# Optimization experiments

Measured on AMD Instinct MI355X. Metric: run time of the kernel, lower is better.

The kernel has to match this reference:

```python
import jax, jax.numpy as jnp
import numpy as np

# Each of the 16 differentiable binary logic ops op_k(a,b) is a polynomial
# c0 + ca*a + cb*b + cab*(a*b). Rows follow the standard difflogic op table
# (op 3 = 'a' pass-through, matching the residual init in the source).
_OP2POLY = np.array([
    [0, 0, 0, 0],    # 0: False
    [0, 0, 0, 1],    # 1: a AND b
    [0, 1, 0, -1],   # 2: a AND NOT b
    [0, 1, 0, 0],    # 3: a
    [0, 0, 1, -1],   # 4: NOT a AND b
    [0, 0, 1, 0],    # 5: b
    [0, 1, 1, -2],   # 6: XOR
    [0, 1, 1, -1],   # 7: OR
    [1, -1, -1, 1],  # 8: NOR
    [1, -1, -1, 2],  # 9: XNOR
    [1, 0, -1, 0],   # 10: NOT b
    [1, 0, -1, 1],   # 11: a OR NOT b
    [1, -1, 0, 0],   # 12: NOT a
    [1, -1, 0, 1],   # 13: NOT a OR b
    [1, 0, 0, -1],   # 14: NAND
    [1, 0, 0, 0],    # 15: True
], dtype=np.float32)

KERNEL_SIZE, STRIDE, PADDING, GROUPS, TREE_DEPTH, TAU = 3, 1, 1, 1, 4, 1.0


def setup_inputs() -> dict:
    key = jax.random.key(0)
    k0, k1, k2, k3, k4 = jax.random.split(key, 5)
    B, Cin, H, W = 16, 64, 64, 64
    OC, N = 128, 2 ** TREE_DEPTH
    x = jax.random.uniform(k0, (B, Cin, H, W), dtype=jnp.float32)
    weights = jax.random.normal(k1, (OC, N - 1, 16), dtype=jnp.float32)
    ci = jax.random.randint(k2, (OC, N), 0, Cin // GROUPS, dtype=jnp.int32)
    px = jax.random.randint(k3, (OC, N), 0, KERNEL_SIZE, dtype=jnp.int32)
    py = jax.random.randint(k4, (OC, N), 0, KERNEL_SIZE, dtype=jnp.int32)
    return {"x": x, "weights": weights, "input_channel_indices": ci,
            "input_pos_x_indices": px, "input_pos_y_indices": py}


def _forward(x, weights, ci, px, py):
    B, Cin, H, W = x.shape
    OC = weights.shape[0]
    N = 2 ** TREE_DEPTH
    # Training-mode weights with straight-through estimator:
    # value = one_hot(argmax), gradient flows through softmax.
    w_soft = jax.nn.softmax(weights / TAU, axis=-1).astype(x.dtype)
    w_hard = jax.nn.one_hot(jnp.argmax(weights, axis=-1), 16, dtype=x.dtype)
    w = w_soft + jax.lax.stop_gradient(w_hard - w_soft)
    # [OC, num_gates, 4] polynomial coefficients over (1, a, b, ab)
    coeffs = jnp.einsum('ogk,kc->ogc', w, jnp.asarray(_OP2POLY, x.dtype))

    xp = jnp.pad(x, ((0, 0), (0, 0), (PADDING, PADDING), (PADDING, PADDING)))
    oh = (H + 2 * PADDING - KERNEL_SIZE) // STRIDE + 1
    ow = (W + 2 * PADDING - KERNEL_SIZE) // STRIDE + 1

    icpg = Cin // GROUPS
    group_of_oc = jnp.arange(OC, dtype=jnp.int32) // (OC // GROUPS)
    chan = group_of_oc[:, None] * icpg + ci                       # [OC, N]
    rows = (jnp.arange(oh, dtype=jnp.int32) * STRIDE)[None, None, :] + py[:, :, None]  # [OC,N,oh]
    cols = (jnp.arange(ow, dtype=jnp.int32) * STRIDE)[None, None, :] + px[:, :, None]  # [OC,N,ow]
    # Irregular per-output gather: [B, OC, N, oh, ow]
    vals = xp[:, chan[:, :, None, None], rows[:, :, :, None], cols[:, :, None, :]]

    # Binary tree of logic gates, level by level (gates stored leaf-level first).
    gate_off = 0
    for _ in range(TREE_DEPTH):
        n = vals.shape[2] // 2
        a, b = vals[:, :, 0::2], vals[:, :, 1::2]
        cc = coeffs[:, gate_off:gate_off + n]                     # [OC, n, 4]
        c0, ca, cb, cab = (cc[None, :, :, i, None, None] for i in range(4))
        vals = c0 + ca * a + cb * b + cab * (a * b)
        gate_off += n
    y = vals[:, :, 0]                                             # [B, OC, oh, ow]

    # 2x2 OR-pool (soft OR = 1 - prod(1 - v)), floor division of spatial dims.
    ph, pw = oh // 2, ow // 2
    y = y[:, :, :ph * 2, :pw * 2].reshape(B, OC, ph, 2, pw, 2)
    return 1.0 - jnp.prod(1.0 - y, axis=(3, 5))


def reference(x, weights, input_channel_indices, input_pos_x_indices, input_pos_y_indices):
    return _forward(x, weights, input_channel_indices, input_pos_x_indices, input_pos_y_indices)
```

## Files before the change

kernel.cpp:

```cpp
#include <hip/hip_runtime.h>

#define BATCH 16
#define CIN   64
#define H_    64
#define W_    64
#define IMG   (H_ * W_)
#define OCH   128
#define NLEAF 16
#define NGATE 15
#define PH    32
#define PW    32

#define ROWS   6
#define RSTR   66
#define CHSTR  (ROWS * RSTR)
#define XSB    2
#define OPS_F  25348
#define DS_F   (OPS_F + OCH * 4)
#define SMEM_F (DS_F + OCH * NLEAF)

typedef float f4v __attribute__((ext_vector_type(4)));

__device__ __constant__ __align__(16) float OP2POLY[16][4] = {
    {0, 0, 0, 0}, {0, 0, 0, 1}, {0, 1, 0, -1}, {0, 1, 0, 0},
    {0, 0, 1, -1}, {0, 0, 1, 0}, {0, 1, 1, -2}, {0, 1, 1, -1},
    {1, -1, -1, 1}, {1, -1, -1, 2}, {1, 0, -1, 0}, {1, 0, -1, 1},
    {1, -1, 0, 0}, {1, -1, 0, 1}, {1, 0, 0, -1}, {1, 0, 0, 0}};

static __device__ __forceinline__ int rfl_i(int v) {
    return __builtin_amdgcn_readfirstlane(v);
}

__global__ __launch_bounds__(1024, 4) void logic_tree_fused(
    const float* __restrict__ x,
    const float* __restrict__ weights,
    const int* __restrict__ ci,
    const int* __restrict__ px,
    const int* __restrict__ py,
    float* __restrict__ out)
{
    __shared__ float smem[SMEM_F];
    int* smem_i = (int*)smem;
    unsigned char* smem_b = (unsigned char*)smem;

    const int blk = blockIdx.x;
    const int xcd = blk & 7;
    const int j   = blk >> 3;
    const int b   = (xcd << 1) | (j >> 4);
    const int strip = j & 15;
    const int r0  = strip << 2;
    const int tid = threadIdx.x;

    const float2* xb2 =
        reinterpret_cast<const float2*>(x + (size_t)b * (CIN * IMG));
#pragma unroll
    for (int i = 0; i < 12; ++i) {
        int f   = tid + i * 1024;
        int ch  = f / 192;
        int rem = f - ch * 192;
        int row = rem >> 5;
        int c2  = rem & 31;
        int gr  = r0 - 1 + row;
        float2 val = make_float2(0.f, 0.f);
        if ((unsigned)gr < (unsigned)H_)
            val = xb2[((ch << 6) | gr) * 32 + c2];
        *reinterpret_cast<float2*>(&smem[XSB + ch * CHSTR + row * RSTR + c2 * 2]) = val;
    }
    if (tid < 770) {
        int idx = (tid < 768) ? (XSB + (tid >> 1) * RSTR + 64 + (tid & 1))
                              : (tid - 768);
        smem[idx] = 0.0f;
    }
    for (int t = tid; t < OCH * NGATE; t += 1024) {
        const float4* wp4 = reinterpret_cast<const float4*>(weights + t * 16);
        const float4 a0 = wp4[0], a1 = wp4[1], a2 = wp4[2], a3 = wp4[3];
        const float wv[16] = {a0.x, a0.y, a0.z, a0.w, a1.x, a1.y, a1.z, a1.w,
                              a2.x, a2.y, a2.z, a2.w, a3.x, a3.y, a3.z, a3.w};
        int best = 0;
        float bv = wv[0];
#pragma unroll
        for (int k = 1; k < 16; ++k)
            if (wv[k] > bv) { bv = wv[k]; best = k; }
        int oc = t / 15, g = t - oc * 15;
        smem_b[OPS_F * 4 + oc * 16 + g] = (unsigned char)best;
        if (g == 14) smem_b[OPS_F * 4 + oc * 16 + 15] = 0;
    }
    for (int t = tid; t < OCH * NLEAF; t += 1024)
        smem_i[DS_F + t] = XSB + ci[t] * CHSTR + py[t] * RSTR + px[t] - 1;
    __syncthreads();

    const int wave = tid >> 6;
    const int lane = tid & 63;
    const size_t obase0 =
        (((size_t)b * OCH) * PH + (strip << 1) + (lane & 1)) * PW + (lane >> 1);

#pragma unroll 1
    for (int q = 0; q < 8; ++q) {
        const int oc = wave * 8 + q;

        const uint4 opsv = *reinterpret_cast<const uint4*>(&smem[OPS_F + oc * 4]);
        const unsigned ou[4] = {
            (unsigned)rfl_i((int)opsv.x), (unsigned)rfl_i((int)opsv.y),
            (unsigned)rfl_i((int)opsv.z), (unsigned)rfl_i((int)opsv.w)};

        int base[NLEAF];
        const int4* D4 = reinterpret_cast<const int4*>(smem_i + DS_F + oc * NLEAF);
#pragma unroll
        for (int m = 0; m < 4; ++m) {
            const int4 d = D4[m];
            base[4 * m + 0] = d.x + lane;
            base[4 * m + 1] = d.y + lane;
            base[4 * m + 2] = d.z + lane;
            base[4 * m + 3] = d.w + lane;
        }

        f4v v[NLEAF];
#pragma unroll
        for (int n = 0; n < NLEAF; ++n) {
            v[n].x = smem[base[n]];
            v[n].y = smem[base[n] + RSTR];
            v[n].z = smem[base[n] + 2 * RSTR];
            v[n].w = smem[base[n] + 3 * RSTR];
        }

        int go = 0;
#pragma unroll
        for (int lev = 8; lev >= 1; lev >>= 1) {
#pragma unroll
            for (int t = 0; t < lev; ++t) {
                const int g  = go + t;
                const int op = (int)((ou[g >> 2] >> ((g & 3) * 8)) & 255u);
                const float4 cc = reinterpret_cast<const float4*>(OP2POLY)[op];
                f4v a  = v[2 * t];
                f4v bb = v[2 * t + 1];
                v[t] = cc.x + cc.y * a + cc.z * bb + cc.w * (a * bb);
            }
            go += lev;
        }

        float p0 = (1.0f - v[0].x) * (1.0f - v[0].y);
        float p1 = (1.0f - v[0].z) * (1.0f - v[0].w);
        float q0 = p0 * __shfl_xor(p0, 1, 64);
        float q1 = p1 * __shfl_xor(p1, 1, 64);
        float val = (lane & 1) ? (1.0f - q1) : (1.0f - q0);
        out[obase0 + (size_t)oc * (PH * PW)] = val;
    }
}

extern "C" void kernel_launch(void* const* d_in, const int* in_sizes, int n_in,
                              void* d_out, int out_size, void* d_ws, size_t ws_size,
                              hipStream_t stream) {
    const float* x       = (const float*)d_in[0];
    const float* weights = (const float*)d_in[1];
    const int*   ci      = (const int*)d_in[2];
    const int*   px      = (const int*)d_in[3];
    const int*   py      = (const int*)d_in[4];
    float* out = (float*)d_out;
    (void)d_ws; (void)ws_size;

    logic_tree_fused<<<BATCH * 16, 1024, 0, stream>>>(x, weights, ci, px, py, out);
}
```

Before: 91.96 us.

## Halve row strip per block and double grid with 512-thread blocks

Each block now computes a 2-row output strip (one pooled row) instead of 4, so it stages 4 input rows per channel instead of 6 and needs less LDS. The grid doubles to 512 blocks of 512 threads, and each wave handles 16 output channels with 2-element vectors. This raises block count and occupancy at the cost of more redundant halo loads and repeated weight argmax decoding per block. Only even lanes write output, which halves the store width.

After: 96.56 us. +5.0%, slower.

```diff
diff --git a/kernel.cpp b/kernel.cpp
--- a/kernel.cpp
+++ b/kernel.cpp
@@ -11,15 +11,15 @@
 #define PH    32
 #define PW    32
 
-#define ROWS   6
+#define SROWS  4
 #define RSTR   66
-#define CHSTR  (ROWS * RSTR)
+#define CHSTR  (SROWS * RSTR)
 #define XSB    2
-#define OPS_F  25348
+#define OPS_F  16900
 #define DS_F   (OPS_F + OCH * 4)
 #define SMEM_F (DS_F + OCH * NLEAF)
 
-typedef float f4v __attribute__((ext_vector_type(4)));
+typedef float f2 __attribute__((ext_vector_type(2)));
 
 __device__ __constant__ __align__(16) float OP2POLY[16][4] = {
     {0, 0, 0, 0}, {0, 0, 0, 1}, {0, 1, 0, -1}, {0, 1, 0, 0},
@@ -31,7 +31,7 @@
     return __builtin_amdgcn_readfirstlane(v);
 }
 
-__global__ __launch_bounds__(1024, 4) void logic_tree_fused(
+__global__ __launch_bounds__(512, 4) void logic_tree_fused(
     const float* __restrict__ x,
     const float* __restrict__ weights,
     const int* __restrict__ ci,
@@ -46,57 +46,62 @@
     const int blk = blockIdx.x;
     const int xcd = blk & 7;
     const int j   = blk >> 3;
-    const int b   = (xcd << 1) | (j >> 4);
-    const int strip = j & 15;
-    const int r0  = strip << 2;
+    const int b   = (xcd << 1) | (j >> 5);
+    const int strip = j & 31;
+    const int r0  = strip << 1;
     const int tid = threadIdx.x;
 
     const float2* xb2 =
         reinterpret_cast<const float2*>(x + (size_t)b * (CIN * IMG));
 #pragma unroll
-    for (int i = 0; i < 12; ++i) {
-        int f   = tid + i * 1024;
-        int ch  = f / 192;
-        int rem = f - ch * 192;
-        int row = rem >> 5;
-        int c2  = rem & 31;
-        int gr  = r0 - 1 + row;
-        float2 val = make_float2(0.f, 0.f);
-        if ((unsigned)gr < (unsigned)H_)
-            val = xb2[((ch << 6) | gr) * 32 + c2];
-        *reinterpret_cast<float2*>(&smem[XSB + ch * CHSTR + row * RSTR + c2 * 2]) = val;
+    for (int i = 0; i < 17; ++i) {
+        int f = tid + i * 512;
+        if (f < 8448) {
+            int ch  = f / 132;
+            int rem = f - ch * 132;
+            int row = rem / 33;
+            int c2  = rem - row * 33;
+            int gr  = r0 - 1 + row;
+            float2 val = make_float2(0.f, 0.f);
+            if (c2 < 32 && (unsigned)gr < (unsigned)H_)
+                val = xb2[((ch << 6) | gr) * 32 + c2];
+            *reinterpret_cast<float2*>(
+                &smem[XSB + ch * CHSTR + row * RSTR + c2 * 2]) = val;
+        }
     }
-    if (tid < 770) {
-        int idx = (tid < 768) ? (XSB + (tid >> 1) * RSTR + 64 + (tid & 1))
-                              : (tid - 768);
-        smem[idx] = 0.0f;
+    if (tid < 2) smem[tid] = 0.0f;
+
+#pragma unroll
+    for (int i = 0; i < 4; ++i) {
+        int t = tid + i * 512;
+        if (t < OCH * NGATE) {
+            const float4* wp4 = reinterpret_cast<const float4*>(weights + t * 16);
+            const float4 a0 = wp4[0], a1 = wp4[1], a2 = wp4[2], a3 = wp4[3];
+            const float wv[16] = {a0.x, a0.y, a0.z, a0.w, a1.x, a1.y, a1.z, a1.w,
+                                  a2.x, a2.y, a2.z, a2.w, a3.x, a3.y, a3.z, a3.w};
+            int best = 0;
+            float bv = wv[0];
+#pragma unroll
+            for (int k = 1; k < 16; ++k)
+                if (wv[k] > bv) { bv = wv[k]; best = k; }
+            int oc = t / 15, g = t - oc * 15;
+            smem_b[OPS_F * 4 + oc * 16 + g] = (unsigned char)best;
+            if (g == 14) smem_b[OPS_F * 4 + oc * 16 + 15] = 0;
+        }
     }
-    for (int t = tid; t < OCH * NGATE; t += 1024) {
-        const float4* wp4 = reinterpret_cast<const float4*>(weights + t * 16);
-        const float4 a0 = wp4[0], a1 = wp4[1], a2 = wp4[2], a3 = wp4[3];
-        const float wv[16] = {a0.x, a0.y, a0.z, a0.w, a1.x, a1.y, a1.z, a1.w,
-                              a2.x, a2.y, a2.z, a2.w, a3.x, a3.y, a3.z, a3.w};
-        int best = 0;
-        float bv = wv[0];
 #pragma unroll
-        for (int k = 1; k < 16; ++k)
-            if (wv[k] > bv) { bv = wv[k]; best = k; }
-        int oc = t / 15, g = t - oc * 15;
-        smem_b[OPS_F * 4 + oc * 16 + g] = (unsigned char)best;
-        if (g == 14) smem_b[OPS_F * 4 + oc * 16 + 15] = 0;
+    for (int i = 0; i < 4; ++i) {
+        int t = tid + i * 512;
+        smem_i[DS_F + t] = XSB + ci[t] * CHSTR + py[t] * RSTR + px[t] - 1;
     }
-    for (int t = tid; t < OCH * NLEAF; t += 1024)
-        smem_i[DS_F + t] = XSB + ci[t] * CHSTR + py[t] * RSTR + px[t] - 1;
     __syncthreads();
 
     const int wave = tid >> 6;
     const int lane = tid & 63;
-    const size_t obase0 =
-        (((size_t)b * OCH) * PH + (strip << 1) + (lane & 1)) * PW + (lane >> 1);
 
 #pragma unroll 1
-    for (int q = 0; q < 8; ++q) {
-        const int oc = wave * 8 + q;
+    for (int q = 0; q < 16; ++q) {
+        const int oc = wave * 16 + q;
 
         const uint4 opsv = *reinterpret_cast<const uint4*>(&smem[OPS_F + oc * 4]);
         const unsigned ou[4] = {
@@ -114,13 +119,11 @@
             base[4 * m + 3] = d.w + lane;
         }
 
-        f4v v[NLEAF];
+        f2 v[NLEAF];
 #pragma unroll
         for (int n = 0; n < NLEAF; ++n) {
             v[n].x = smem[base[n]];
             v[n].y = smem[base[n] + RSTR];
-            v[n].z = smem[base[n] + 2 * RSTR];
-            v[n].w = smem[base[n] + 3 * RSTR];
         }
 
         int go = 0;
@@ -131,19 +134,18 @@
                 const int g  = go + t;
                 const int op = (int)((ou[g >> 2] >> ((g & 3) * 8)) & 255u);
                 const float4 cc = reinterpret_cast<const float4*>(OP2POLY)[op];
-                f4v a  = v[2 * t];
-                f4v bb = v[2 * t + 1];
+                f2 a  = v[2 * t];
+                f2 bb = v[2 * t + 1];
                 v[t] = cc.x + cc.y * a + cc.z * bb + cc.w * (a * bb);
             }
             go += lev;
         }
 
-        float p0 = (1.0f - v[0].x) * (1.0f - v[0].y);
-        float p1 = (1.0f - v[0].z) * (1.0f - v[0].w);
-        float q0 = p0 * __shfl_xor(p0, 1, 64);
-        float q1 = p1 * __shfl_xor(p1, 1, 64);
-        float val = (lane & 1) ? (1.0f - q1) : (1.0f - q0);
-        out[obase0 + (size_t)oc * (PH * PW)] = val;
+        float p  = (1.0f - v[0].x) * (1.0f - v[0].y);
+        float pp = p * __shfl_xor(p, 1, 64);
+        if (!(lane & 1))
+            out[(((size_t)b * OCH + oc) * PH + strip) * PW + (lane >> 1)] =
+                1.0f - pp;
     }
 }
 
@@ -158,5 +160,5 @@
     float* out = (float*)d_out;
     (void)d_ws; (void)ws_size;
 
-    logic_tree_fused<<<BATCH * 16, 1024, 0, stream>>>(x, weights, ci, px, py, out);
+    logic_tree_fused<<<BATCH * 32, 512, 0, stream>>>(x, weights, ci, px, py, out);
 }
```
